# Optimization experiments

Hardware: AMD Instinct MI355X
Metric: run time of the kernel (lower is better)

The kernel has to match this reference:

```python
import jax, jax.numpy as jnp
import numpy as np

N_NODES = 100000
N_EDGES = 1600000
N_FEAT = 128
HIDDEN = 64
N_CLASSES = 16


def setup_inputs() -> dict:
    key = jax.random.key(0)
    ks = jax.random.split(key, 8)
    x = jax.random.normal(ks[0], (N_NODES, N_FEAT), dtype=jnp.float32)
    edge_index = jax.random.randint(ks[1], (2, N_EDGES), 0, N_NODES, dtype=jnp.int64)
    def glorot(k, shape):
        lim = float(np.sqrt(6.0 / (shape[0] + shape[1])))
        return jax.random.uniform(k, shape, jnp.float32, -lim, lim)
    return {
        "x": x,
        "edge_index": edge_index,
        "W0": glorot(ks[2], (N_FEAT, HIDDEN)), "b0": jnp.zeros((HIDDEN,), jnp.float32),
        "W1": glorot(ks[3], (HIDDEN, HIDDEN)), "b1": jnp.zeros((HIDDEN,), jnp.float32),
        "W2": glorot(ks[4], (HIDDEN, 2)),      "b2": jnp.zeros((2,), jnp.float32),
        "Wc": glorot(ks[5], (2, N_CLASSES)),   "bc": jnp.zeros((N_CLASSES,), jnp.float32),
    }


def _gcn_conv(x, W, b, src, dst, norm, n_nodes):
    # GCNConv: D^{-1/2} (A + I) D^{-1/2} X W + b, edges already include self-loops
    h = x @ W                                  # transform first (small dim)
    msg = h[src] * norm[:, None]               # gather + per-edge scale
    agg = jax.ops.segment_sum(msg, dst, num_segments=n_nodes)  # scatter-add
    return agg + b


def reference(x, edge_index, W0, b0, W1, b1, W2, b2, Wc, bc):
    n = x.shape[0]
    loops = jnp.arange(n, dtype=edge_index.dtype)
    src = jnp.concatenate([edge_index[0], loops])
    dst = jnp.concatenate([edge_index[1], loops])
    # degree on destination (col), including self-loops
    deg = jax.ops.segment_sum(jnp.ones_like(dst, dtype=x.dtype), dst, num_segments=n)
    dis = jnp.where(deg > 0, jax.lax.rsqrt(deg), 0.0)
    norm = dis[src] * dis[dst]

    h = _gcn_conv(x, W0, b0, src, dst, norm, n)              # layer 0, no activation
    h = jnp.tanh(_gcn_conv(h, W1, b1, src, dst, norm, n))    # layer 1
    h = jnp.tanh(_gcn_conv(h, W2, b2, src, dst, norm, n))    # layer 2 -> [N, 2]
    embeddings = h
    out = embeddings @ Wc + bc                               # [N, num_classes]
    return (out, embeddings)
```

## Files before the change

### kernel.cpp

```cpp
#include <hip/hip_runtime.h>


#define NF 128
#define NH 64
#define NPB 256
#define MAXNB 512
#define CAP 6144
#define A1G 512

typedef _Float16 half8 __attribute__((ext_vector_type(8)));
typedef float f32x4 __attribute__((ext_vector_type(4)));

__global__ void k_prep0(const float* __restrict__ W0, const float* __restrict__ W1,
                        short* __restrict__ wf0, short* __restrict__ wf1,
                        const int* __restrict__ ei, int* __restrict__ fmt,
                        int* __restrict__ ccnt, int nb16) {
    int b = blockIdx.x;
    int t = threadIdx.x;
    if (b < 24) {
        int lane = t & 63;
        int j0 = (t >> 6) * 2;
        const float* W = (b < 16) ? W0 : W1;
        int bb = (b < 16) ? b : (b - 16);
        short* wf = (b < 16) ? wf0 : wf1;
        int lohalf = (b < 16) ? 8192 : 4096;
        int kc = bb >> 2, ct = bb & 3;
        #pragma unroll
        for (int jj = 0; jj < 2; ++jj) {
            int j = j0 + jj;
            int k = kc * 32 + (lane >> 4) * 8 + j;
            int col = ct * 16 + (lane & 15);
            float w = W[k * NH + col];
            _Float16 h = (_Float16)w;
            _Float16 l = (_Float16)(w - (float)h);
            int idx = (bb * 64 + lane) * 8 + j;
            wf[idx] = *(short*)&h;
            wf[idx + lohalf] = *(short*)&l;
        }
        return;
    }
    int i = (b - 24) * 256 + t;
    if (i < nb16) ccnt[i] = 0;
    if (i == 0) {
        int f = 1;
        #pragma unroll
        for (int k = 1; k < 32; k += 2) if (ei[k] != 0) f = 0;
        *fmt = f;
    }
}

__global__ void __launch_bounds__(256) k_coarse(
        const int* __restrict__ ei, const int* __restrict__ fmt,
        int* __restrict__ ccnt, int* __restrict__ blockbase, int E, int NB) {
    __shared__ int h[MAXNB];
    int sh = *fmt;
    for (int i = threadIdx.x; i < NB; i += 256) h[i] = 0;
    __syncthreads();
    const long long S = (long long)A1G * 256;
    long long e = (long long)blockIdx.x * 256 + threadIdx.x;
    for (; e + 3 * S < E; e += 4 * S) {
        int d0 = ei[(long long)(E + e) << sh];
        int d1 = ei[(long long)(E + e + S) << sh];
        int d2 = ei[(long long)(E + e + 2 * S) << sh];
        int d3 = ei[(long long)(E + e + 3 * S) << sh];
        atomicAdd(&h[d0 >> 8], 1);
        atomicAdd(&h[d1 >> 8], 1);
        atomicAdd(&h[d2 >> 8], 1);
        atomicAdd(&h[d3 >> 8], 1);
    }
    for (; e < E; e += S) {
        int d = ei[(long long)(E + e) << sh];
        atomicAdd(&h[d >> 8], 1);
    }
    __syncthreads();
    for (int b = threadIdx.x; b < NB; b += 256) {
        int c = h[b];
        int base = (c > 0) ? atomicAdd(&ccnt[b * 16], c) : 0;
        blockbase[(long long)blockIdx.x * NB + b] = base;
    }
}

__global__ void __launch_bounds__(512) k_cscan(
        const int* __restrict__ ccnt, int* __restrict__ cstart, int NB) {
    __shared__ int s[512];
    int t = threadIdx.x;
    int c = (t < NB) ? ccnt[t * 16] : 0;
    s[t] = c;
    __syncthreads();
    for (int off = 1; off < 512; off <<= 1) {
        int v = s[t];
        int u = (t >= off) ? s[t - off] : 0;
        __syncthreads();
        s[t] = v + u;
        __syncthreads();
    }
    if (t < NB) cstart[t] = s[t] - c;
}

__global__ void __launch_bounds__(256) k_cscatter(
        const int* __restrict__ ei, const int* __restrict__ fmt,
        const int* __restrict__ cstart, const int* __restrict__ blockbase,
        int* __restrict__ pairs, int E, int NB) {
    __shared__ int h[MAXNB];
    __shared__ int bb[MAXNB];
    int sh = *fmt;
    for (int i = threadIdx.x; i < NB; i += 256) {
        h[i] = 0;
        bb[i] = cstart[i] + blockbase[(long long)blockIdx.x * NB + i];
    }
    __syncthreads();
    const long long S = (long long)A1G * 256;
    long long e = (long long)blockIdx.x * 256 + threadIdx.x;
    for (; e + 3 * S < E; e += 4 * S) {
        int s0 = ei[(long long)e << sh];
        int s1 = ei[(long long)(e + S) << sh];
        int s2 = ei[(long long)(e + 2 * S) << sh];
        int s3 = ei[(long long)(e + 3 * S) << sh];
        int d0 = ei[(long long)(E + e) << sh];
        int d1 = ei[(long long)(E + e + S) << sh];
        int d2 = ei[(long long)(E + e + 2 * S) << sh];
        int d3 = ei[(long long)(E + e + 3 * S) << sh];
        int b0 = d0 >> 8, b1 = d1 >> 8, b2 = d2 >> 8, b3 = d3 >> 8;
        int r0 = atomicAdd(&h[b0], 1);
        pairs[bb[b0] + r0] = s0 | ((d0 & 255) << 17);
        int r1 = atomicAdd(&h[b1], 1);
        pairs[bb[b1] + r1] = s1 | ((d1 & 255) << 17);
        int r2 = atomicAdd(&h[b2], 1);
        pairs[bb[b2] + r2] = s2 | ((d2 & 255) << 17);
        int r3 = atomicAdd(&h[b3], 1);
        pairs[bb[b3] + r3] = s3 | ((d3 & 255) << 17);
    }
    for (; e < E; e += S) {
        int s = ei[(long long)e << sh];
        int d = ei[(long long)(E + e) << sh];
        int b = d >> 8;
        int r = atomicAdd(&h[b], 1);
        pairs[bb[b] + r] = s | ((d & 255) << 17);
    }
}

__global__ void __launch_bounds__(256) k_bucket(
        const int* __restrict__ pairs, const int* __restrict__ ccnt,
        const int* __restrict__ cstart, int* __restrict__ esrc,
        int* __restrict__ cnt, int* __restrict__ start, float* __restrict__ dis,
        int N) {
    __shared__ int words[CAP];
    __shared__ unsigned char rk[CAP];
    __shared__ int h[NPB];
    __shared__ int hs[NPB];
    int b = blockIdx.x;
    int cs = cstart[b];
    int ec = ccnt[b * 16];
    if (ec > CAP) ec = CAP;
    int t = threadIdx.x;
    for (int i = t; i < ec; i += 256) words[i] = pairs[cs + i];
    h[t] = 0;
    __syncthreads();
    for (int i = t; i < ec; i += 256) {
        int ld = words[i] >> 17;
        rk[i] = (unsigned char)atomicAdd(&h[ld], 1);
    }
    __syncthreads();
    int c = h[t];
    hs[t] = c;
    __syncthreads();
    for (int off = 1; off < 256; off <<= 1) {
        int v = hs[t];
        int u = (t >= off) ? hs[t - off] : 0;
        __syncthreads();
        hs[t] = v + u;
        __syncthreads();
    }
    int node = b * NPB + t;
    if (node < N) {
        cnt[node] = c;
        start[node] = cs + hs[t] - c;
        dis[node] = rsqrtf(1.0f + (float)c);
    }
    for (int i = t; i < ec; i += 256) {
        int w = words[i];
        int ld = w >> 17;
        esrc[cs + (hs[ld] - h[ld]) + rk[i]] = w & 0x1FFFF;
    }
}

#define GEMM_EPILOGUE                                                         \
    int rb = (int)rowbase + wid * 16 + (lane >> 4) * 4;                       \
    float drs[4];                                                             \
    drs[0] = (rb + 0 < n) ? dis[rb + 0] : 0.0f;                               \
    drs[1] = (rb + 1 < n) ? dis[rb + 1] : 0.0f;                               \
    drs[2] = (rb + 2 < n) ? dis[rb + 2] : 0.0f;                               \
    drs[3] = (rb + 3 < n) ? dis[rb + 3] : 0.0f;                               \
    const float ks = 1.0f / 32767.0f;                                         \
    int cb = lane & 15;                                                       \
    _Pragma("unroll")                                                         \
    for (int r = 0; r < 4; ++r) {                                             \
        float v0 = acc0[r] * drs[r];                                          \
        float v1 = acc1[r] * drs[r];                                          \
        float v2 = acc2[r] * drs[r];                                          \
        float v3 = acc3[r] * drs[r];                                          \
        float m = fmaxf(fmaxf(fabsf(v0), fabsf(v1)), fmaxf(fabsf(v2), fabsf(v3))); \
        m = fmaxf(m, __shfl_xor(m, 1, 64));                                   \
        m = fmaxf(m, __shfl_xor(m, 2, 64));                                   \
        m = fmaxf(m, __shfl_xor(m, 4, 64));                                   \
        m = fmaxf(m, __shfl_xor(m, 8, 64));                                   \
        float ir = 32767.0f / fmaxf(m, 1e-20f);                               \
        int rowg = rb + r;                                                    \
        if (rowg < n) {                                                       \
            long long base = (long long)rowg * NH;                            \
            T16[base + 0  + cb] = (short)__float2int_rn(v0 * ir);             \
            T16[base + 16 + cb] = (short)__float2int_rn(v1 * ir);             \
            T16[base + 32 + cb] = (short)__float2int_rn(v2 * ir);             \
            T16[base + 48 + cb] = (short)__float2int_rn(v3 * ir);             \
            if (cb == 0) rs[rowg] = m * ks;                                   \
        }                                                                     \
    }

#define CVT_AFRAG(xa, xb4)                                                    \
    half8 ah, al;                                                             \
    {                                                                         \
        float xv[8] = {xa.x, xa.y, xa.z, xa.w, xb4.x, xb4.y, xb4.z, xb4.w};   \
        _Pragma("unroll")                                                     \
        for (int e = 0; e < 8; ++e) {                                         \
            _Float16 h = (_Float16)xv[e];                                     \
            ah[e] = h;                                                        \
            al[e] = (_Float16)(xv[e] - (float)h);                             \
        }                                                                     \
    }

#define MFMA3(ACC, SETIDX, LOHALF)                                            \
    {                                                                         \
        const half8 bh = *(const half8*)&Wf[((SETIDX) * 64 + lane) * 8];      \
        const half8 bl = *(const half8*)&Wf[((SETIDX) * 64 + lane) * 8 + (LOHALF)]; \
        ACC = __builtin_amdgcn_mfma_f32_16x16x32_f16(ah, bh, ACC, 0, 0, 0);   \
        ACC = __builtin_amdgcn_mfma_f32_16x16x32_f16(ah, bl, ACC, 0, 0, 0);   \
        ACC = __builtin_amdgcn_mfma_f32_16x16x32_f16(al, bh, ACC, 0, 0, 0);   \
    }

__global__ void __launch_bounds__(256) k_gemmM(
        const float* __restrict__ X, const short* __restrict__ wfrag,
        const float* __restrict__ dis, short* __restrict__ T16,
        float* __restrict__ rs, int n) {
    __shared__ __align__(16) short Wf[16384];
    int tid = threadIdx.x;
    {
        const int4* src = (const int4*)wfrag;
        int4* dst = (int4*)Wf;
        #pragma unroll
        for (int u = 0; u < 8; ++u) dst[tid + u * 256] = src[tid + u * 256];
    }
    __syncthreads();
    long long rowbase = (long long)blockIdx.x * 64;
    int lane = tid & 63;
    int wid = tid >> 6;
    int row = (int)rowbase + wid * 16 + (lane & 15);
    bool ok = row < n;
    const float* xb = X + (long long)row * NF + (lane >> 4) * 8;
    f32x4 acc0 = {0,0,0,0}, acc1 = {0,0,0,0}, acc2 = {0,0,0,0}, acc3 = {0,0,0,0};
    #pragma unroll
    for (int kc = 0; kc < 4; ++kc) {
        float4 xa = ok ? *(const float4*)(xb + kc * 32)
                       : make_float4(0.f, 0.f, 0.f, 0.f);
        float4 xc = ok ? *(const float4*)(xb + kc * 32 + 4)
                       : make_float4(0.f, 0.f, 0.f, 0.f);
        CVT_AFRAG(xa, xc)
        MFMA3(acc0, kc * 4 + 0, 8192)
        MFMA3(acc1, kc * 4 + 1, 8192)
        MFMA3(acc2, kc * 4 + 2, 8192)
        MFMA3(acc3, kc * 4 + 3, 8192)
    }
    GEMM_EPILOGUE
}

__global__ void __launch_bounds__(256) k_gemmM64(
        const float* __restrict__ H, const short* __restrict__ wfrag,
        const float* __restrict__ dis, short* __restrict__ T16,
        float* __restrict__ rs, int n) {
    __shared__ __align__(16) short Wf[8192];
    int tid = threadIdx.x;
    {
        const int4* src = (const int4*)wfrag;
        int4* dst = (int4*)Wf;
        #pragma unroll
        for (int u = 0; u < 4; ++u) dst[tid + u * 256] = src[tid + u * 256];
    }
    __syncthreads();
    long long rowbase = (long long)blockIdx.x * 64;
    int lane = tid & 63;
    int wid = tid >> 6;
    int row = (int)rowbase + wid * 16 + (lane & 15);
    bool ok = row < n;
    const float* hb = H + (long long)row * NH + (lane >> 4) * 8;
    f32x4 acc0 = {0,0,0,0}, acc1 = {0,0,0,0}, acc2 = {0,0,0,0}, acc3 = {0,0,0,0};
    #pragma unroll
    for (int kc = 0; kc < 2; ++kc) {
        float4 xa = ok ? *(const float4*)(hb + kc * 32)
                       : make_float4(0.f, 0.f, 0.f, 0.f);
        float4 xc = ok ? *(const float4*)(hb + kc * 32 + 4)
                       : make_float4(0.f, 0.f, 0.f, 0.f);
        CVT_AFRAG(xa, xc)
        MFMA3(acc0, kc * 4 + 0, 4096)
        MFMA3(acc1, kc * 4 + 1, 4096)
        MFMA3(acc2, kc * 4 + 2, 4096)
        MFMA3(acc3, kc * 4 + 3, 4096)
    }
    GEMM_EPILOGUE
}

#define EDGE_A(J) {                                                           \
    int s_ = __builtin_amdgcn_readlane(sA, (J));                              \
    float f_ = __int_as_float(__builtin_amdgcn_readlane(fAb, (J)));           \
    accA = fmaf(f_, (float)(T + s_ * NH)[lane], accA); }
#define EDGE_B(J) {                                                           \
    int s_ = __builtin_amdgcn_readlane(sB, (J));                              \
    float f_ = __int_as_float(__builtin_amdgcn_readlane(fBb, (J)));           \
    accB = fmaf(f_, (float)(T + s_ * NH)[lane], accB); }

#define SEG_GATHER2                                                           \
    int lane = threadIdx.x & 63;                                              \
    int na = blockIdx.x * 8 + (threadIdx.x >> 6) * 2;                         \
    int nb_ = na + 1;                                                         \
    if (na >= n) return;                                                      \
    bool hasB = (nb_ < n);                                                    \
    float dia = dis[na];                                                      \
    float dib = hasB ? dis[nb_] : 0.0f;                                       \
    int ga = cnt[na], sta = start[na];                                        \
    int gb = hasB ? cnt[nb_] : 0;                                             \
    int stb = hasB ? start[nb_] : 0;                                          \
    float accA = rs[na] * (float)T[na * NH + lane];                           \
    float accB = hasB ? rs[nb_] * (float)T[nb_ * NH + lane] : 0.0f;           \
    int gmax = ga > gb ? ga : gb;                                             \
    for (int base = 0; base < gmax; base += 64) {                             \
        int ma = ga - base; ma = ma < 0 ? 0 : (ma > 64 ? 64 : ma);            \
        int mb = gb - base; mb = mb < 0 ? 0 : (mb > 64 ? 64 : mb);            \
        int sA = 0, sB = 0; float fA = 0.0f, fB = 0.0f;                       \
        if (lane < ma) { sA = esrc[sta + base + lane]; fA = rs[sA]; }         \
        if (lane < mb) { sB = esrc[stb + base + lane]; fB = rs[sB]; }         \
        int fAb = __float_as_int(fA), fBb = __float_as_int(fB);               \
        int mmin = ma < mb ? ma : mb;                                         \
        int j = 0;                                                            \
        for (; j + 3 < mmin; j += 4) {                                        \
            EDGE_A(j + 0) EDGE_B(j + 0)                                       \
            EDGE_A(j + 1) EDGE_B(j + 1)                                       \
            EDGE_A(j + 2) EDGE_B(j + 2)                                       \
            EDGE_A(j + 3) EDGE_B(j + 3)                                       \
        }                                                                     \
        int jA = j, jB = j;                                                   \
        for (; jA + 3 < ma; jA += 4) {                                        \
            EDGE_A(jA + 0) EDGE_A(jA + 1) EDGE_A(jA + 2) EDGE_A(jA + 3)       \
        }                                                                     \
        for (; jA < ma; ++jA) EDGE_A(jA)                                      \
        for (; jB + 3 < mb; jB += 4) {                                        \
            EDGE_B(jB + 0) EDGE_B(jB + 1) EDGE_B(jB + 2) EDGE_B(jB + 3)       \
        }                                                                     \
        for (; jB < mb; ++jB) EDGE_B(jB)                                      \
    }

__global__ void __launch_bounds__(256) k_seg(
        const short* __restrict__ T, const float* __restrict__ rs,
        const int* __restrict__ esrc, const int* __restrict__ start,
        const int* __restrict__ cnt, const float* __restrict__ dis,
        const float* __restrict__ b0, float* __restrict__ O, int n) {
    SEG_GATHER2
    float bv = b0[lane];
    O[(long long)na * NH + lane] = dia * accA + bv;
    if (hasB) O[(long long)nb_ * NH + lane] = dib * accB + bv;
}

__global__ void __launch_bounds__(256) k_seg1f(
        const short* __restrict__ T, const float* __restrict__ rs,
        const int* __restrict__ esrc, const int* __restrict__ start,
        const int* __restrict__ cnt, const float* __restrict__ dis,
        const float* __restrict__ b1, const float* __restrict__ W2,
        float2* __restrict__ t2, int n) {
    SEG_GATHER2
    float bv = b1[lane];
    float2 w = ((const float2*)W2)[lane];
    float tA = tanhf(dia * accA + bv);
    float p0 = tA * w.x, p1 = tA * w.y;
    float tB = hasB ? tanhf(dib * accB + bv) : 0.0f;
    float q0 = tB * w.x, q1 = tB * w.y;
    #pragma unroll
    for (int msk = 32; msk; msk >>= 1) {
        p0 += __shfl_xor(p0, msk, 64);
        p1 += __shfl_xor(p1, msk, 64);
        q0 += __shfl_xor(q0, msk, 64);
        q1 += __shfl_xor(q1, msk, 64);
    }
    if (lane == 0) {
        t2[na] = make_float2(dia * p0, dia * p1);
        if (hasB) t2[nb_] = make_float2(dib * q0, dib * q1);
    }
}

__global__ void __launch_bounds__(256) k_seg2f(
        const float2* __restrict__ T2, const int* __restrict__ esrc,
        const int* __restrict__ start, const int* __restrict__ cnt,
        const float* __restrict__ dis, const float* __restrict__ b2,
        const float* __restrict__ Wc, const float* __restrict__ bc,
        float* __restrict__ out, float* __restrict__ emb, int n) {
    int lane = threadIdx.x & 63;
    int sub = lane >> 4;
    int sl = lane & 15;
    int i = blockIdx.x * 16 + (threadIdx.x >> 6) * 4 + sub;
    if (i >= n) return;
    float di = dis[i];
    int g = cnt[i], st = start[i];
    float a0 = 0.0f, a1 = 0.0f;
    for (int j = sl; j < g; j += 16) {
        float2 v = T2[esrc[st + j]];
        a0 += v.x; a1 += v.y;
    }
    if (sl == 0) {
        float2 s = T2[i];
        a0 += s.x; a1 += s.y;
    }
    #pragma unroll
    for (int msk = 8; msk; msk >>= 1) {
        a0 += __shfl_xor(a0, msk, 64);
        a1 += __shfl_xor(a1, msk, 64);
    }
    float e0 = tanhf(a0 * di + b2[0]);
    float e1 = tanhf(a1 * di + b2[1]);
    if (sl == 0) *(float2*)&emb[(long long)i * 2] = make_float2(e0, e1);
    if (sl < 4) {
        int c = sl * 4;
        float4 o;
        o.x = e0 * Wc[c + 0] + e1 * Wc[16 + c + 0] + bc[c + 0];
        o.y = e0 * Wc[c + 1] + e1 * Wc[16 + c + 1] + bc[c + 1];
        o.z = e0 * Wc[c + 2] + e1 * Wc[16 + c + 2] + bc[c + 2];
        o.w = e0 * Wc[c + 3] + e1 * Wc[16 + c + 3] + bc[c + 3];
        *(float4*)&out[(long long)i * 16 + c] = o;
    }
}

extern "C" void kernel_launch(void* const* d_in, const int* in_sizes, int n_in,
                              void* d_out, int out_size, void* d_ws, size_t ws_size,
                              hipStream_t stream) {
    const float* x  = (const float*)d_in[0];
    const int*   ei = (const int*)  d_in[1];
    const float* W0 = (const float*)d_in[2];
    const float* b0 = (const float*)d_in[3];
    const float* W1 = (const float*)d_in[4];
    const float* b1 = (const float*)d_in[5];
    const float* W2 = (const float*)d_in[6];
    const float* b2 = (const float*)d_in[7];
    const float* Wc = (const float*)d_in[8];
    const float* bc = (const float*)d_in[9];

    int N = in_sizes[0] / NF;
    int E = in_sizes[1] / 2;
    int NB = (N + NPB - 1) / NPB;

    float* out = (float*)d_out;
    float* emb = out + (long long)N * 16;

    short*  T16a = (short*)d_ws;
    float*  Bb   = (float*)((char*)d_ws + (long long)N * NH * 2);
    float*  dis  = (float*)((char*)d_ws + (long long)N * NH * 2 + (long long)N * NH * 4);
    float*  rs_a = dis + N;
    int*    cnt   = (int*)(rs_a + N);
    int*    start = cnt + N;
    int*    esrc  = start + N;
    int*    fmt   = esrc + E;
    short*  wf0   = (short*)d_out;
    short*  wf1   = wf0 + 16384;
    float2* t2    = (float2*)Bb;

    int* pairs     = (int*)d_ws;
    int* blockbase = pairs + E;
    int* ccnt      = blockbase + (long long)A1G * NB;
    int* cstart    = ccnt + NB * 16;

    int nb_g  = (N + 63) / 64;
    int nb_s2 = (N + 7) / 8;
    int nb_2f = (N + 15) / 16;
    int nb16  = NB * 16;
    int nb_i0 = (nb16 + 255) / 256;

    k_prep0   <<<24 + nb_i0, 256, 0, stream>>>(W0, W1, wf0, wf1, ei, fmt,
                                               ccnt, nb16);
    k_coarse  <<<A1G, 256, 0, stream>>>(ei, fmt, ccnt, blockbase, E, NB);
    k_cscan   <<<1, 512, 0, stream>>>(ccnt, cstart, NB);
    k_cscatter<<<A1G, 256, 0, stream>>>(ei, fmt, cstart, blockbase, pairs, E, NB);
    k_bucket  <<<NB, 256, 0, stream>>>(pairs, ccnt, cstart, esrc, cnt, start, dis, N);

    k_gemmM   <<<nb_g, 256, 0, stream>>>(x, wf0, dis, T16a, rs_a, N);

    k_seg     <<<nb_s2, 256, 0, stream>>>(T16a, rs_a, esrc, start, cnt, dis, b0,
                                          Bb, N);

    k_gemmM64 <<<nb_g, 256, 0, stream>>>(Bb, wf1, dis, T16a, rs_a, N);

    k_seg1f   <<<nb_s2, 256, 0, stream>>>(T16a, rs_a, esrc, start, cnt, dis, b1,
                                          W2, t2, N);

    k_seg2f   <<<nb_2f, 256, 0, stream>>>(t2, esrc, start, cnt, dis, b2, Wc, bc,
                                          out, emb, N);
}
```

Baseline: 277.4 us.

## Fuse coarse histogram with layer-0 GEMM and defer degree scaling to bucket

Merges the coarse destination histogram kernel and the first-layer GEMM into one launch, so the edge-counting blocks and the GEMM blocks run at the same time. Because the GEMM now runs before degrees are known, its epilogue quantizes the unscaled rows, and the per-row scale is multiplied by the inverse square root of the degree later in the bucket kernel. This is exact because the scale is per row. The sort scratch buffers are moved into the Bb buffer. Shared memory per block for the combined kernel is fixed at 32KB, which may lower occupancy for the histogram blocks.

```diff
diff --git a/kernel.cpp b/kernel.cpp
--- a/kernel.cpp
+++ b/kernel.cpp
@@ -49,140 +49,32 @@
     }
 }
 
-__global__ void __launch_bounds__(256) k_coarse(
-        const int* __restrict__ ei, const int* __restrict__ fmt,
-        int* __restrict__ ccnt, int* __restrict__ blockbase, int E, int NB) {
-    __shared__ int h[MAXNB];
-    int sh = *fmt;
-    for (int i = threadIdx.x; i < NB; i += 256) h[i] = 0;
-    __syncthreads();
-    const long long S = (long long)A1G * 256;
-    long long e = (long long)blockIdx.x * 256 + threadIdx.x;
-    for (; e + 3 * S < E; e += 4 * S) {
-        int d0 = ei[(long long)(E + e) << sh];
-        int d1 = ei[(long long)(E + e + S) << sh];
-        int d2 = ei[(long long)(E + e + 2 * S) << sh];
-        int d3 = ei[(long long)(E + e + 3 * S) << sh];
-        atomicAdd(&h[d0 >> 8], 1);
-        atomicAdd(&h[d1 >> 8], 1);
-        atomicAdd(&h[d2 >> 8], 1);
-        atomicAdd(&h[d3 >> 8], 1);
-    }
-    for (; e < E; e += S) {
-        int d = ei[(long long)(E + e) << sh];
-        atomicAdd(&h[d >> 8], 1);
-    }
-    __syncthreads();
-    for (int b = threadIdx.x; b < NB; b += 256) {
-        int c = h[b];
-        int base = (c > 0) ? atomicAdd(&ccnt[b * 16], c) : 0;
-        blockbase[(long long)blockIdx.x * NB + b] = base;
-    }
-}
-
-__global__ void __launch_bounds__(512) k_cscan(
-        const int* __restrict__ ccnt, int* __restrict__ cstart, int NB) {
-    __shared__ int s[512];
-    int t = threadIdx.x;
-    int c = (t < NB) ? ccnt[t * 16] : 0;
-    s[t] = c;
-    __syncthreads();
-    for (int off = 1; off < 512; off <<= 1) {
-        int v = s[t];
-        int u = (t >= off) ? s[t - off] : 0;
-        __syncthreads();
-        s[t] = v + u;
-        __syncthreads();
-    }
-    if (t < NB) cstart[t] = s[t] - c;
-}
-
-__global__ void __launch_bounds__(256) k_cscatter(
-        const int* __restrict__ ei, const int* __restrict__ fmt,
-        const int* __restrict__ cstart, const int* __restrict__ blockbase,
-        int* __restrict__ pairs, int E, int NB) {
-    __shared__ int h[MAXNB];
-    __shared__ int bb[MAXNB];
-    int sh = *fmt;
-    for (int i = threadIdx.x; i < NB; i += 256) {
-        h[i] = 0;
-        bb[i] = cstart[i] + blockbase[(long long)blockIdx.x * NB + i];
-    }
-    __syncthreads();
-    const long long S = (long long)A1G * 256;
-    long long e = (long long)blockIdx.x * 256 + threadIdx.x;
-    for (; e + 3 * S < E; e += 4 * S) {
-        int s0 = ei[(long long)e << sh];
-        int s1 = ei[(long long)(e + S) << sh];
-        int s2 = ei[(long long)(e + 2 * S) << sh];
-        int s3 = ei[(long long)(e + 3 * S) << sh];
-        int d0 = ei[(long long)(E + e) << sh];
-        int d1 = ei[(long long)(E + e + S) << sh];
-        int d2 = ei[(long long)(E + e + 2 * S) << sh];
-        int d3 = ei[(long long)(E + e + 3 * S) << sh];
-        int b0 = d0 >> 8, b1 = d1 >> 8, b2 = d2 >> 8, b3 = d3 >> 8;
-        int r0 = atomicAdd(&h[b0], 1);
-        pairs[bb[b0] + r0] = s0 | ((d0 & 255) << 17);
-        int r1 = atomicAdd(&h[b1], 1);
-        pairs[bb[b1] + r1] = s1 | ((d1 & 255) << 17);
-        int r2 = atomicAdd(&h[b2], 1);
-        pairs[bb[b2] + r2] = s2 | ((d2 & 255) << 17);
-        int r3 = atomicAdd(&h[b3], 1);
-        pairs[bb[b3] + r3] = s3 | ((d3 & 255) << 17);
-    }
-    for (; e < E; e += S) {
-        int s = ei[(long long)e << sh];
-        int d = ei[(long long)(E + e) << sh];
-        int b = d >> 8;
-        int r = atomicAdd(&h[b], 1);
-        pairs[bb[b] + r] = s | ((d & 255) << 17);
-    }
-}
-
-__global__ void __launch_bounds__(256) k_bucket(
-        const int* __restrict__ pairs, const int* __restrict__ ccnt,
-        const int* __restrict__ cstart, int* __restrict__ esrc,
-        int* __restrict__ cnt, int* __restrict__ start, float* __restrict__ dis,
-        int N) {
-    __shared__ int words[CAP];
-    __shared__ unsigned char rk[CAP];
-    __shared__ int h[NPB];
-    __shared__ int hs[NPB];
-    int b = blockIdx.x;
-    int cs = cstart[b];
-    int ec = ccnt[b * 16];
-    if (ec > CAP) ec = CAP;
-    int t = threadIdx.x;
-    for (int i = t; i < ec; i += 256) words[i] = pairs[cs + i];
-    h[t] = 0;
-    __syncthreads();
-    for (int i = t; i < ec; i += 256) {
-        int ld = words[i] >> 17;
-        rk[i] = (unsigned char)atomicAdd(&h[ld], 1);
-    }
-    __syncthreads();
-    int c = h[t];
-    hs[t] = c;
-    __syncthreads();
-    for (int off = 1; off < 256; off <<= 1) {
-        int v = hs[t];
-        int u = (t >= off) ? hs[t - off] : 0;
-        __syncthreads();
-        hs[t] = v + u;
-        __syncthreads();
-    }
-    int node = b * NPB + t;
-    if (node < N) {
-        cnt[node] = c;
-        start[node] = cs + hs[t] - c;
-        dis[node] = rsqrtf(1.0f + (float)c);
-    }
-    for (int i = t; i < ec; i += 256) {
-        int w = words[i];
-        int ld = w >> 17;
-        esrc[cs + (hs[ld] - h[ld]) + rk[i]] = w & 0x1FFFF;
-    }
-}
+#define GEMM_EPILOGUE_RAW                                                     \
+    int rb = (int)rowbase + wid * 16 + (lane >> 4) * 4;                       \
+    const float ks = 1.0f / 32767.0f;                                         \
+    int cb = lane & 15;                                                       \
+    _Pragma("unroll")                                                         \
+    for (int r = 0; r < 4; ++r) {                                             \
+        float v0 = acc0[r];                                                   \
+        float v1 = acc1[r];                                                   \
+        float v2 = acc2[r];                                                   \
+        float v3 = acc3[r];                                                   \
+        float m = fmaxf(fmaxf(fabsf(v0), fabsf(v1)), fmaxf(fabsf(v2), fabsf(v3))); \
+        m = fmaxf(m, __shfl_xor(m, 1, 64));                                   \
+        m = fmaxf(m, __shfl_xor(m, 2, 64));                                   \
+        m = fmaxf(m, __shfl_xor(m, 4, 64));                                   \
+        m = fmaxf(m, __shfl_xor(m, 8, 64));                                   \
+        float ir = 32767.0f / fmaxf(m, 1e-20f);                               \
+        int rowg = rb + r;                                                    \
+        if (rowg < n) {                                                       \
+            long long base = (long long)rowg * NH;                            \
+            T16[base + 0  + cb] = (short)__float2int_rn(v0 * ir);             \
+            T16[base + 16 + cb] = (short)__float2int_rn(v1 * ir);             \
+            T16[base + 32 + cb] = (short)__float2int_rn(v2 * ir);             \
+            T16[base + 48 + cb] = (short)__float2int_rn(v3 * ir);             \
+            if (cb == 0) rs[rowg] = m * ks;                                   \
+        }                                                                     \
+    }
 
 #define GEMM_EPILOGUE                                                         \
     int rb = (int)rowbase + wid * 16 + (lane >> 4) * 4;                       \
@@ -237,12 +129,43 @@
         ACC = __builtin_amdgcn_mfma_f32_16x16x32_f16(al, bh, ACC, 0, 0, 0);   \
     }
 
-__global__ void __launch_bounds__(256) k_gemmM(
+__global__ void __launch_bounds__(256) k_pre_g(
+        const int* __restrict__ ei, const int* __restrict__ fmt,
+        int* __restrict__ ccnt, int* __restrict__ blockbase, int E, int NB,
         const float* __restrict__ X, const short* __restrict__ wfrag,
-        const float* __restrict__ dis, short* __restrict__ T16,
-        float* __restrict__ rs, int n) {
-    __shared__ __align__(16) short Wf[16384];
+        short* __restrict__ T16, float* __restrict__ rs, int n) {
+    __shared__ __align__(16) char smem[32768];
     int tid = threadIdx.x;
+    if (blockIdx.x < A1G) {
+        int* h = (int*)smem;
+        int sh = *fmt;
+        for (int i = tid; i < NB; i += 256) h[i] = 0;
+        __syncthreads();
+        const long long S = (long long)A1G * 256;
+        long long e = (long long)blockIdx.x * 256 + tid;
+        for (; e + 3 * S < E; e += 4 * S) {
+            int d0 = ei[(long long)(E + e) << sh];
+            int d1 = ei[(long long)(E + e + S) << sh];
+            int d2 = ei[(long long)(E + e + 2 * S) << sh];
+            int d3 = ei[(long long)(E + e + 3 * S) << sh];
+            atomicAdd(&h[d0 >> 8], 1);
+            atomicAdd(&h[d1 >> 8], 1);
+            atomicAdd(&h[d2 >> 8], 1);
+            atomicAdd(&h[d3 >> 8], 1);
+        }
+        for (; e < E; e += S) {
+            int d = ei[(long long)(E + e) << sh];
+            atomicAdd(&h[d >> 8], 1);
+        }
+        __syncthreads();
+        for (int b = tid; b < NB; b += 256) {
+            int c = h[b];
+            int base = (c > 0) ? atomicAdd(&ccnt[b * 16], c) : 0;
+            blockbase[(long long)blockIdx.x * NB + b] = base;
+        }
+        return;
+    }
+    short* Wf = (short*)smem;
     {
         const int4* src = (const int4*)wfrag;
         int4* dst = (int4*)Wf;
@@ -250,7 +173,7 @@
         for (int u = 0; u < 8; ++u) dst[tid + u * 256] = src[tid + u * 256];
     }
     __syncthreads();
-    long long rowbase = (long long)blockIdx.x * 64;
+    long long rowbase = (long long)(blockIdx.x - A1G) * 64;
     int lane = tid & 63;
     int wid = tid >> 6;
     int row = (int)rowbase + wid * 16 + (lane & 15);
@@ -269,7 +192,113 @@
         MFMA3(acc2, kc * 4 + 2, 8192)
         MFMA3(acc3, kc * 4 + 3, 8192)
     }
-    GEMM_EPILOGUE
+    GEMM_EPILOGUE_RAW
+}
+
+__global__ void __launch_bounds__(512) k_cscan(
+        const int* __restrict__ ccnt, int* __restrict__ cstart, int NB) {
+    __shared__ int s[512];
+    int t = threadIdx.x;
+    int c = (t < NB) ? ccnt[t * 16] : 0;
+    s[t] = c;
+    __syncthreads();
+    for (int off = 1; off < 512; off <<= 1) {
+        int v = s[t];
+        int u = (t >= off) ? s[t - off] : 0;
+        __syncthreads();
+        s[t] = v + u;
+        __syncthreads();
+    }
+    if (t < NB) cstart[t] = s[t] - c;
+}
+
+__global__ void __launch_bounds__(256) k_cscatter(
+        const int* __restrict__ ei, const int* __restrict__ fmt,
+        const int* __restrict__ cstart, const int* __restrict__ blockbase,
+        int* __restrict__ pairs, int E, int NB) {
+    __shared__ int h[MAXNB];
+    __shared__ int bb[MAXNB];
+    int sh = *fmt;
+    for (int i = threadIdx.x; i < NB; i += 256) {
+        h[i] = 0;
+        bb[i] = cstart[i] + blockbase[(long long)blockIdx.x * NB + i];
+    }
+    __syncthreads();
+    const long long S = (long long)A1G * 256;
+    long long e = (long long)blockIdx.x * 256 + threadIdx.x;
+    for (; e + 3 * S < E; e += 4 * S) {
+        int s0 = ei[(long long)e << sh];
+        int s1 = ei[(long long)(e + S) << sh];
+        int s2 = ei[(long long)(e + 2 * S) << sh];
+        int s3 = ei[(long long)(e + 3 * S) << sh];
+        int d0 = ei[(long long)(E + e) << sh];
+        int d1 = ei[(long long)(E + e + S) << sh];
+        int d2 = ei[(long long)(E + e + 2 * S) << sh];
+        int d3 = ei[(long long)(E + e + 3 * S) << sh];
+        int b0 = d0 >> 8, b1 = d1 >> 8, b2 = d2 >> 8, b3 = d3 >> 8;
+        int r0 = atomicAdd(&h[b0], 1);
+        pairs[bb[b0] + r0] = s0 | ((d0 & 255) << 17);
+        int r1 = atomicAdd(&h[b1], 1);
+        pairs[bb[b1] + r1] = s1 | ((d1 & 255) << 17);
+        int r2 = atomicAdd(&h[b2], 1);
+        pairs[bb[b2] + r2] = s2 | ((d2 & 255) << 17);
+        int r3 = atomicAdd(&h[b3], 1);
+        pairs[bb[b3] + r3] = s3 | ((d3 & 255) << 17);
+    }
+    for (; e < E; e += S) {
+        int s = ei[(long long)e << sh];
+        int d = ei[(long long)(E + e) << sh];
+        int b = d >> 8;
+        int r = atomicAdd(&h[b], 1);
+        pairs[bb[b] + r] = s | ((d & 255) << 17);
+    }
+}
+
+__global__ void __launch_bounds__(256) k_bucket(
+        const int* __restrict__ pairs, const int* __restrict__ ccnt,
+        const int* __restrict__ cstart, int* __restrict__ esrc,
+        int* __restrict__ cnt, int* __restrict__ start, float* __restrict__ dis,
+        float* __restrict__ rs, int N) {
+    __shared__ int words[CAP];
+    __shared__ unsigned char rk[CAP];
+    __shared__ int h[NPB];
+    __shared__ int hs[NPB];
+    int b = blockIdx.x;
+    int cs = cstart[b];
+    int ec = ccnt[b * 16];
+    if (ec > CAP) ec = CAP;
+    int t = threadIdx.x;
+    for (int i = t; i < ec; i += 256) words[i] = pairs[cs + i];
+    h[t] = 0;
+    __syncthreads();
+    for (int i = t; i < ec; i += 256) {
+        int ld = words[i] >> 17;
+        rk[i] = (unsigned char)atomicAdd(&h[ld], 1);
+    }
+    __syncthreads();
+    int c = h[t];
+    hs[t] = c;
+    __syncthreads();
+    for (int off = 1; off < 256; off <<= 1) {
+        int v = hs[t];
+        int u = (t >= off) ? hs[t - off] : 0;
+        __syncthreads();
+        hs[t] = v + u;
+        __syncthreads();
+    }
+    int node = b * NPB + t;
+    if (node < N) {
+        float di = rsqrtf(1.0f + (float)c);
+        cnt[node] = c;
+        start[node] = cs + hs[t] - c;
+        dis[node] = di;
+        rs[node] *= di;
+    }
+    for (int i = t; i < ec; i += 256) {
+        int w = words[i];
+        int ld = w >> 17;
+        esrc[cs + (hs[ld] - h[ld]) + rk[i]] = w & 0x1FFFF;
+    }
 }
 
 __global__ void __launch_bounds__(256) k_gemmM64(
@@ -478,14 +507,19 @@
     int nb16  = NB * 16;
     int nb_i0 = (nb16 + 255) / 256;
 
+    pairs     = (int*)Bb;
+    blockbase = pairs + E;
+    ccnt      = blockbase + (long long)A1G * NB;
+    cstart    = ccnt + NB * 16;
+
     k_prep0   <<<24 + nb_i0, 256, 0, stream>>>(W0, W1, wf0, wf1, ei, fmt,
                                                ccnt, nb16);
-    k_coarse  <<<A1G, 256, 0, stream>>>(ei, fmt, ccnt, blockbase, E, NB);
+    k_pre_g   <<<A1G + nb_g, 256, 0, stream>>>(ei, fmt, ccnt, blockbase, E, NB,
+                                               x, wf0, T16a, rs_a, N);
     k_cscan   <<<1, 512, 0, stream>>>(ccnt, cstart, NB);
     k_cscatter<<<A1G, 256, 0, stream>>>(ei, fmt, cstart, blockbase, pairs, E, NB);
-    k_bucket  <<<NB, 256, 0, stream>>>(pairs, ccnt, cstart, esrc, cnt, start, dis, N);
-
-    k_gemmM   <<<nb_g, 256, 0, stream>>>(x, wf0, dis, T16a, rs_a, N);
+    k_bucket  <<<NB, 256, 0, stream>>>(pairs, ccnt, cstart, esrc, cnt, start,
+                                       dis, rs_a, N);
 
     k_seg     <<<nb_s2, 256, 0, stream>>>(T16a, rs_a, esrc, start, cnt, dis, b0,
                                           Bb, N);
```

New measurement: 278.9 us. No clear change (+0.6%).
